# Kernel optimization log

Measured on AMD Instinct MI355X. Metric: run time of the kernel, lower is better.

## Reference

```python
import jax, jax.numpy as jnp
import numpy as np
from jax import lax

# Module config (matches init_kwargs)
B, CIN, COUT, H, W = 64, 128, 256, 64, 64
K, STRIDE, PAD = 4, 2, 1
POOL_K, POOL_S = 2, 2
HT_MIN, HT_MAX = -1.0, 1.0


def setup_inputs() -> dict:
    key = jax.random.key(0)
    k1, k2, k3 = jax.random.split(key, 3)
    x = jax.random.normal(k1, (B, CIN, H, W), dtype=jnp.float32)
    # torch ConvTranspose2d default init scale ~ 1/sqrt(Cin*K*K)
    scale = 1.0 / np.sqrt(CIN * K * K)
    weight = jax.random.normal(k2, (CIN, COUT, K, K), dtype=jnp.float32) * scale
    bias = jax.random.normal(k3, (COUT,), dtype=jnp.float32) * scale
    return {"x": x, "weight": weight, "bias": bias}


def reference(x, weight, bias):
    # ConvTranspose2d(stride=2, padding=1): equivalent forward conv with
    # lhs_dilation=stride, flipped kernel, padding k-1-p on each side.
    w = jnp.flip(weight, axis=(2, 3)).transpose(1, 0, 2, 3)  # (Cout, Cin, K, K)
    pad = K - 1 - PAD
    y = lax.conv_general_dilated(
        x, w,
        window_strides=(1, 1),
        padding=[(pad, pad), (pad, pad)],
        lhs_dilation=(STRIDE, STRIDE),
        dimension_numbers=("NCHW", "OIHW", "NCHW"),
    ) + bias[None, :, None, None]  # [B, Cout, 128, 128]

    # MaxPool2d(kernel=2, stride=2), VALID
    y = lax.reduce_window(
        y, -jnp.inf, lax.max,
        window_dimensions=(1, 1, POOL_K, POOL_K),
        window_strides=(1, 1, POOL_S, POOL_S),
        padding="VALID",
    )  # [B, Cout, 64, 64]

    # Hardtanh -> spatial mean (keepdim) -> Tanh
    y = jnp.clip(y, HT_MIN, HT_MAX)
    y = jnp.mean(y, axis=(2, 3), keepdims=True)  # [B, Cout, 1, 1]
    return jnp.tanh(y)
```

## Files before the change

kernel.cpp:

```cpp
#include <hip/hip_runtime.h>
#include <hip/hip_bf16.h>
#include <cstdint>


typedef __attribute__((ext_vector_type(8))) short short8;
typedef __attribute__((ext_vector_type(4))) float f32x4;

__device__ __forceinline__ void async16(const void* g, void* l) {
  __builtin_amdgcn_global_load_lds(
      reinterpret_cast<const unsigned int __attribute__((address_space(1)))*>(
          reinterpret_cast<uintptr_t>(g)),
      reinterpret_cast<unsigned int __attribute__((address_space(3)))*>(
          reinterpret_cast<uintptr_t>(l)),
      16, 0, 0);
}

__device__ __forceinline__ unsigned short f2bf(float f) {
  union { float f; unsigned int u; } v; v.f = f;
  unsigned int u = v.u;
  return (unsigned short)((u + 0x7fffu + ((u >> 16) & 1u)) >> 16);
}

__device__ __forceinline__ short8 and_mask(short8 v, unsigned m) {
  union { short8 s; unsigned u[4]; } x;
  x.s = v;
  x.u[0] &= m; x.u[1] &= m; x.u[2] &= m; x.u[3] &= m;
  return x.s;
}

__global__ __launch_bounds__(256) void k_xpose(const float* __restrict__ x,
                                               unsigned short* __restrict__ xT) {
  __shared__ float tile[64][132];
  int bid = blockIdx.x;
  int b = bid >> 6, h = bid & 63;
  const float* src = x + (size_t)b * 524288 + h * 64;
  int w = threadIdx.x & 63, cg = threadIdx.x >> 6;
#pragma unroll
  for (int cc = 0; cc < 32; ++cc) {
    int cin = cc * 4 + cg;
    tile[w][cin] = src[(size_t)cin * 4096 + w];
  }
  __syncthreads();
  unsigned short* dst = xT + (size_t)(b * 64 + h) * 8192;
#pragma unroll
  for (int it = 0; it < 4; ++it) {
    int e = it * 2048 + threadIdx.x * 8;
    int ww = e >> 7, cin = e & 127;
    unsigned int pk[4];
#pragma unroll
    for (int j = 0; j < 4; ++j) {
      unsigned int lo = f2bf(tile[ww][cin + 2 * j]);
      unsigned int hi = f2bf(tile[ww][cin + 2 * j + 1]);
      pk[j] = lo | (hi << 16);
    }
    *reinterpret_cast<uint4*>(dst + e) = make_uint4(pk[0], pk[1], pk[2], pk[3]);
  }
}

__global__ __launch_bounds__(256) void k_wpack(const float* __restrict__ w,
                                               unsigned short* __restrict__ wT) {
  int o = blockIdx.x * 256 + threadIdx.x;
  int cin = o & 127;
  int cout = (o >> 7) & 255;
  int khkw = o >> 15;
  int kh = khkw >> 2, kw = khkw & 3;
  float f = w[((size_t)cin * 256 + cout) * 16 + kh * 4 + kw];
  wT[o] = f2bf(f);
}

#define XS_B     98304
#define WBUF_SZ  32768
#define LDS_TOTAL 163840

__global__ __launch_bounds__(512, 2) void k_main(
    const unsigned short* __restrict__ xT,
    const unsigned short* __restrict__ wT,
    const float* __restrict__ bias,
    float* __restrict__ acc) {
  extern __shared__ char smem[];
  const int bid = blockIdx.x;
  const int nt  = bid & 1;
  const int prg = (bid >> 1) & 15;
  const int b   = bid >> 5;
  const int n0  = nt * 128;
  const int tid  = threadIdx.x;
  const int lane = tid & 63;
  const int wid  = tid >> 6;
  const int wm   = wid >> 1;
  const int wn   = wid & 1;
  const int l15  = lane & 15;

  {
    const char* xTb = (const char*)xT + (size_t)b * 1048576;
#pragma unroll
    for (int it = 0; it < 12; ++it) {
      const int gbase = wid * 12288 + it * 1024;
      const int g = gbase + lane * 16;
      const int r = g >> 14;
      const int ir = 4 * prg - 1 + r;
      const int rc = g >> 8;
      const int key = (rc & 7) << 4;
      if ((unsigned)ir < 64u) {
        const int oir = g & 16383;
        const char* src = xTb + ir * 16384 + (oir & ~255) + ((oir & 255) ^ key);
        async16(src, smem + gbase);
      } else {
        *reinterpret_cast<f32x4*>(smem + g) = (f32x4){0.f, 0.f, 0.f, 0.f};
      }
    }
  }

  auto stage_w = [&](int khkw, int buf) {
    char* dstbase = smem + XS_B + buf * WBUF_SZ;
    const char* g0 = (const char*)wT + ((size_t)khkw * 256 + n0) * 256;
#pragma unroll
    for (int it = 0; it < 4; ++it) {
      const int gbase = wid * 4096 + it * 1024;
      const int g = gbase + lane * 16;
      const int cl = g >> 8;
      const int key = (cl & 7) << 4;
      async16(g0 + (g & ~255) + ((g & 255) ^ key), dstbase + gbase);
    }
  };

  const int KHt[2][2] = {{1, 3}, {2, 0}};
  const int DHt[2][2] = {{0, -1}, {0, 1}};
  const unsigned kmneg = (l15 == 0)  ? 0u : ~0u;
  const unsigned kmpos = (l15 == 15) ? 0u : ~0u;

  stage_w(5, 0);
  __syncthreads();

  f32x4 accf[4][4], rm[4][4];
#pragma unroll
  for (int mi = 0; mi < 4; ++mi)
#pragma unroll
    for (int ni = 0; ni < 4; ++ni) accf[mi][ni] = (f32x4){0.f, 0.f, 0.f, 0.f};

  unsigned boff[4]; int bkey[4];
#pragma unroll
  for (int ni = 0; ni < 4; ++ni) {
    int cl = wn * 64 + ni * 16 + l15;
    boff[ni] = cl * 256 + (lane >> 4) * 16;
    bkey[ni] = (cl & 7) << 4;
  }

#pragma unroll
  for (int q = 0; q < 4; ++q) {
    const int qh = q >> 1, qw = q & 1;
#pragma unroll
    for (int t = 0; t < 4; ++t) {
      const int th = t >> 1, tw = t & 1;
      const int idx = q * 4 + t;
      if (idx < 15) {
        const int nidx = idx + 1;
        const int q2 = nidx >> 2, t2 = nidx & 3;
        const int kh2 = KHt[q2 >> 1][t2 >> 1];
        const int kw2 = KHt[q2 & 1][t2 & 1];
        stage_w(kh2 * 4 + kw2, nidx & 1);
      }
      const int dr = DHt[qh][th];
      const int dw = DHt[qw][tw];
      const int ar = wm + 1 + dr;
      unsigned aoff[4]; int akey[4];
#pragma unroll
      for (int mi = 0; mi < 4; ++mi) {
        int col = mi * 16 + l15 + dw;
        int colc = col < 0 ? 0 : (col > 63 ? 63 : col);
        int rc = ar * 64 + colc;
        aoff[mi] = rc * 256 + (lane >> 4) * 16;
        akey[mi] = (rc & 7) << 4;
      }
      char* wb = smem + XS_B + (idx & 1) * WBUF_SZ;
#pragma unroll
      for (int kk = 0; kk < 4; ++kk) {
        short8 a[4], bb[4];
#pragma unroll
        for (int mi = 0; mi < 4; ++mi)
          a[mi] = *reinterpret_cast<const short8*>(smem + ((aoff[mi] + kk * 64) ^ akey[mi]));
        if (dw < 0) a[0] = and_mask(a[0], kmneg);
        if (dw > 0) a[3] = and_mask(a[3], kmpos);
#pragma unroll
        for (int ni = 0; ni < 4; ++ni)
          bb[ni] = *reinterpret_cast<const short8*>(wb + ((boff[ni] + kk * 64) ^ bkey[ni]));
#pragma unroll
        for (int mi = 0; mi < 4; ++mi)
#pragma unroll
          for (int ni = 0; ni < 4; ++ni)
            accf[mi][ni] = __builtin_amdgcn_mfma_f32_16x16x32_bf16(a[mi], bb[ni], accf[mi][ni], 0, 0, 0);
      }
      if (t == 3) {
#pragma unroll
        for (int mi = 0; mi < 4; ++mi)
#pragma unroll
          for (int ni = 0; ni < 4; ++ni) {
            if (q == 0) {
              rm[mi][ni] = accf[mi][ni];
            } else {
#pragma unroll
              for (int rr = 0; rr < 4; ++rr)
                rm[mi][ni][rr] = fmaxf(rm[mi][ni][rr], accf[mi][ni][rr]);
            }
            accf[mi][ni] = (f32x4){0.f, 0.f, 0.f, 0.f};
          }
      }
      __syncthreads();
    }
  }

#pragma unroll
  for (int ni = 0; ni < 4; ++ni) {
    const int cout = n0 + wn * 64 + ni * 16 + l15;
    const float bv = bias[cout];
    float s = 0.f;
#pragma unroll
    for (int mi = 0; mi < 4; ++mi)
#pragma unroll
      for (int rr = 0; rr < 4; ++rr) {
        float v = rm[mi][ni][rr] + bv;
        v = fminf(1.f, fmaxf(-1.f, v));
        s += v;
      }
    s += __shfl_xor(s, 16, 64);
    s += __shfl_xor(s, 32, 64);
    if (lane < 16) atomicAdd(&acc[b * 256 + cout], s);
  }
}

__global__ __launch_bounds__(256) void k_fin(const float* __restrict__ acc,
                                             float* __restrict__ out) {
  int i = blockIdx.x * 256 + threadIdx.x;
  out[i] = tanhf(acc[i] * (1.0f / 4096.0f));
}

extern "C" void kernel_launch(void* const* d_in, const int* in_sizes, int n_in,
                              void* d_out, int out_size, void* d_ws, size_t ws_size,
                              hipStream_t stream) {
  const float* x    = (const float*)d_in[0];
  const float* w    = (const float*)d_in[1];
  const float* bias = (const float*)d_in[2];
  float* out = (float*)d_out;
  char* ws = (char*)d_ws;

  float* acc          = (float*)ws;
  unsigned short* xT  = (unsigned short*)(ws + 65536);
  unsigned short* wT  = (unsigned short*)(ws + 65536 + 67108864);

  hipMemsetAsync(acc, 0, 65536, stream);
  k_xpose<<<4096, 256, 0, stream>>>(x, xT);
  k_wpack<<<2048, 256, 0, stream>>>(w, wT);

  hipFuncSetAttribute(reinterpret_cast<const void*>(k_main),
                      hipFuncAttributeMaxDynamicSharedMemorySize, LDS_TOTAL);
  k_main<<<2048, 512, LDS_TOTAL, stream>>>(xT, wT, bias, acc);
  k_fin<<<64, 256, 0, stream>>>(acc, out);
}
```

Baseline: 424.6 us.

## Load weights directly from global into registers, shrink blocks and LDS

Removes the double-buffered LDS staging of weight tiles and the per-tap __syncthreads, so each wave loads its B fragments straight from global memory (L2-cached) into registers. Blocks shrink from 512 to 256 threads, each covering 2 pooled rows instead of 4, and LDS drops to 64KB, which should raise occupancy and remove barrier stalls. The trade-off is that every wave reads weights separately from global/L2 with no reuse through LDS. It also uses 16 more VGPR-held B fragments per tap, adding register pressure.

Result: slower. 741.4 us (+74.6%).

```diff
diff --git a/kernel.cpp b/kernel.cpp
--- a/kernel.cpp
+++ b/kernel.cpp
@@ -68,20 +68,18 @@
   wT[o] = f2bf(f);
 }
 
-#define XS_B     98304
-#define WBUF_SZ  32768
-#define LDS_TOTAL 163840
-
-__global__ __launch_bounds__(512, 2) void k_main(
+#define LDS_TOTAL 65536
+
+__global__ __launch_bounds__(256, 2) void k_main(
     const unsigned short* __restrict__ xT,
     const unsigned short* __restrict__ wT,
     const float* __restrict__ bias,
     float* __restrict__ acc) {
   extern __shared__ char smem[];
   const int bid = blockIdx.x;
-  const int nt  = bid & 1;
-  const int prg = (bid >> 1) & 15;
-  const int b   = bid >> 5;
+  const int pr  = bid & 31;
+  const int nt  = (bid >> 5) & 1;
+  const int b   = bid >> 6;
   const int n0  = nt * 128;
   const int tid  = threadIdx.x;
   const int lane = tid & 63;
@@ -89,61 +87,41 @@
   const int wm   = wid >> 1;
   const int wn   = wid & 1;
   const int l15  = lane & 15;
+  const int l4   = lane >> 4;
 
   {
     const char* xTb = (const char*)xT + (size_t)b * 1048576;
 #pragma unroll
-    for (int it = 0; it < 12; ++it) {
-      const int gbase = wid * 12288 + it * 1024;
+    for (int it = 0; it < 16; ++it) {
+      const int gbase = it * 4096 + wid * 1024;
       const int g = gbase + lane * 16;
       const int r = g >> 14;
-      const int ir = 4 * prg - 1 + r;
-      const int rc = g >> 8;
-      const int key = (rc & 7) << 4;
+      const int ir = 2 * pr - 1 + r;
       if ((unsigned)ir < 64u) {
-        const int oir = g & 16383;
-        const char* src = xTb + ir * 16384 + (oir & ~255) + ((oir & 255) ^ key);
+        const int rc = g >> 8;
+        const int key = (rc & 7) << 4;
+        const char* src = xTb + ir * 16384 + (rc & 63) * 256 + ((g & 255) ^ key);
         async16(src, smem + gbase);
       } else {
         *reinterpret_cast<f32x4*>(smem + g) = (f32x4){0.f, 0.f, 0.f, 0.f};
       }
     }
   }
-
-  auto stage_w = [&](int khkw, int buf) {
-    char* dstbase = smem + XS_B + buf * WBUF_SZ;
-    const char* g0 = (const char*)wT + ((size_t)khkw * 256 + n0) * 256;
-#pragma unroll
-    for (int it = 0; it < 4; ++it) {
-      const int gbase = wid * 4096 + it * 1024;
-      const int g = gbase + lane * 16;
-      const int cl = g >> 8;
-      const int key = (cl & 7) << 4;
-      async16(g0 + (g & ~255) + ((g & 255) ^ key), dstbase + gbase);
-    }
-  };
+  __syncthreads();
 
   const int KHt[2][2] = {{1, 3}, {2, 0}};
   const int DHt[2][2] = {{0, -1}, {0, 1}};
   const unsigned kmneg = (l15 == 0)  ? 0u : ~0u;
   const unsigned kmpos = (l15 == 15) ? 0u : ~0u;
 
-  stage_w(5, 0);
-  __syncthreads();
-
   f32x4 accf[4][4], rm[4][4];
 #pragma unroll
   for (int mi = 0; mi < 4; ++mi)
 #pragma unroll
     for (int ni = 0; ni < 4; ++ni) accf[mi][ni] = (f32x4){0.f, 0.f, 0.f, 0.f};
 
-  unsigned boff[4]; int bkey[4];
-#pragma unroll
-  for (int ni = 0; ni < 4; ++ni) {
-    int cl = wn * 64 + ni * 16 + l15;
-    boff[ni] = cl * 256 + (lane >> 4) * 16;
-    bkey[ni] = (cl & 7) << 4;
-  }
+  const char* wb0 = (const char*)wT + (size_t)n0 * 256;
+  const int boff = (wn * 64 + l15) * 256 + l4 * 16;
 
 #pragma unroll
   for (int q = 0; q < 4; ++q) {
@@ -151,43 +129,40 @@
 #pragma unroll
     for (int t = 0; t < 4; ++t) {
       const int th = t >> 1, tw = t & 1;
-      const int idx = q * 4 + t;
-      if (idx < 15) {
-        const int nidx = idx + 1;
-        const int q2 = nidx >> 2, t2 = nidx & 3;
-        const int kh2 = KHt[q2 >> 1][t2 >> 1];
-        const int kw2 = KHt[q2 & 1][t2 & 1];
-        stage_w(kh2 * 4 + kw2, nidx & 1);
-      }
+      const int kh = KHt[qh][th], kw = KHt[qw][tw];
+      const char* wb = wb0 + (kh * 4 + kw) * 65536;
+      short8 bb[4][4];
+#pragma unroll
+      for (int ni = 0; ni < 4; ++ni)
+#pragma unroll
+        for (int kk = 0; kk < 4; ++kk)
+          bb[ni][kk] = *reinterpret_cast<const short8*>(wb + boff + ni * 4096 + kk * 64);
+
       const int dr = DHt[qh][th];
       const int dw = DHt[qw][tw];
       const int ar = wm + 1 + dr;
-      unsigned aoff[4]; int akey[4];
+      int aoff[4], akey[4];
 #pragma unroll
       for (int mi = 0; mi < 4; ++mi) {
         int col = mi * 16 + l15 + dw;
         int colc = col < 0 ? 0 : (col > 63 ? 63 : col);
         int rc = ar * 64 + colc;
-        aoff[mi] = rc * 256 + (lane >> 4) * 16;
+        aoff[mi] = rc * 256 + l4 * 16;
         akey[mi] = (rc & 7) << 4;
       }
-      char* wb = smem + XS_B + (idx & 1) * WBUF_SZ;
 #pragma unroll
       for (int kk = 0; kk < 4; ++kk) {
-        short8 a[4], bb[4];
+        short8 a[4];
 #pragma unroll
         for (int mi = 0; mi < 4; ++mi)
           a[mi] = *reinterpret_cast<const short8*>(smem + ((aoff[mi] + kk * 64) ^ akey[mi]));
         if (dw < 0) a[0] = and_mask(a[0], kmneg);
         if (dw > 0) a[3] = and_mask(a[3], kmpos);
 #pragma unroll
-        for (int ni = 0; ni < 4; ++ni)
-          bb[ni] = *reinterpret_cast<const short8*>(wb + ((boff[ni] + kk * 64) ^ bkey[ni]));
-#pragma unroll
         for (int mi = 0; mi < 4; ++mi)
 #pragma unroll
           for (int ni = 0; ni < 4; ++ni)
-            accf[mi][ni] = __builtin_amdgcn_mfma_f32_16x16x32_bf16(a[mi], bb[ni], accf[mi][ni], 0, 0, 0);
+            accf[mi][ni] = __builtin_amdgcn_mfma_f32_16x16x32_bf16(a[mi], bb[ni][kk], accf[mi][ni], 0, 0, 0);
       }
       if (t == 3) {
 #pragma unroll
@@ -204,7 +179,6 @@
             accf[mi][ni] = (f32x4){0.f, 0.f, 0.f, 0.f};
           }
       }
-      __syncthreads();
     }
   }
 
@@ -252,6 +226,6 @@
 
   hipFuncSetAttribute(reinterpret_cast<const void*>(k_main),
                       hipFuncAttributeMaxDynamicSharedMemorySize, LDS_TOTAL);
-  k_main<<<2048, 512, LDS_TOTAL, stream>>>(xT, wT, bias, acc);
+  k_main<<<4096, 256, LDS_TOTAL, stream>>>(xT, wT, bias, acc);
   k_fin<<<64, 256, 0, stream>>>(acc, out);
 }
```
